# Kernel optimization log

Measured on AMD Instinct MI355X. Metric: run time of the kernel, lower is better.

## Reference

```python
import jax, jax.numpy as jnp
import numpy as np

B, N, D = 16, 1024, 5
R_HID = 8  # radial MLP hidden width


def setup_inputs() -> dict:
    key = jax.random.key(0)
    ks = jax.random.split(key, 16)
    feats = jax.random.normal(ks[0], (B, N, D), jnp.float32)
    coors = 3.0 * jax.random.normal(ks[1], (B, N, 3), jnp.float32)
    a = jax.random.bernoulli(ks[2], 0.01, (B, N, N))
    adj_mat = a | jnp.swapaxes(a, 1, 2)
    s = 1.0 / np.sqrt(D)
    Wq = s * jax.random.normal(ks[3], (D, D), jnp.float32)
    Wk = s * jax.random.normal(ks[4], (D, D), jnp.float32)
    Wv = s * jax.random.normal(ks[5], (D, D), jnp.float32)
    Wo = s * jax.random.normal(ks[6], (D, D), jnp.float32)
    w_r1 = 0.5 * jax.random.normal(ks[7], (1, R_HID), jnp.float32)
    b_r1 = jnp.zeros((R_HID,), jnp.float32)
    w_r2 = 0.5 * jax.random.normal(ks[8], (R_HID, 1), jnp.float32)
    b_r2 = jnp.zeros((1,), jnp.float32)
    w1 = (1.0 / np.sqrt(D)) * jax.random.normal(ks[9], (D, 128), jnp.float32)
    b1 = jnp.zeros((128,), jnp.float32)
    w2 = (1.0 / np.sqrt(128.0)) * jax.random.normal(ks[10], (128, 3), jnp.float32)
    b2 = jnp.zeros((3,), jnp.float32)
    return dict(feats=feats, coors=coors, adj_mat=adj_mat, Wq=Wq, Wk=Wk, Wv=Wv,
                Wo=Wo, w_r1=w_r1, b_r1=b_r1, w_r2=w_r2, b_r2=b_r2,
                w1=w1, b1=b1, w2=w2, b2=b2)


def _se3_layer(feats, coors, neigh, Wq, Wk, Wv, Wo, w_r1, b_r1, w_r2, b_r2):
    # SE(3)-invariant sparse graph attention on degree-0 channels.
    # Attention logits = content term + radial (distance-only) bias, so the
    # scalar output is invariant to global rotations/translations of coors.
    q = jnp.einsum('bnd,de->bne', feats, Wq)
    k = jnp.einsum('bnd,de->bne', feats, Wk)
    v = jnp.einsum('bnd,de->bne', feats, Wv)
    rel = coors[:, :, None, :] - coors[:, None, :, :]        # [B,N,N,3]
    dist = jnp.sqrt(jnp.sum(rel * rel, axis=-1) + 1e-8)      # [B,N,N]
    h = jax.nn.relu(dist[..., None] * w_r1[0] + b_r1)        # [B,N,N,R_HID]
    rbias = (h @ w_r2)[..., 0] + b_r2[0]                     # [B,N,N]
    scores = jnp.einsum('bid,bjd->bij', q, k) / np.sqrt(q.shape[-1]) + rbias
    scores = jnp.where(neigh, scores, -1e9)
    attn = jax.nn.softmax(scores, axis=-1)
    agg = jnp.einsum('bij,bjd->bid', attn, v)
    return feats + jnp.einsum('bid,de->bie', agg, Wo)        # residual


def reference(feats, coors, adj_mat, Wq, Wk, Wv, Wo, w_r1, b_r1, w_r2, b_r2,
              w1, b1, w2, b2):
    a = adj_mat.astype(jnp.float32)
    # num_adj_degrees=2: attend over 1-hop and 2-hop neighbors (+ self)
    adj2 = jnp.einsum('bij,bjk->bik', a, a) > 0
    eye = jnp.eye(adj_mat.shape[1], dtype=bool)[None]
    neigh = adj_mat | adj2 | eye
    x = _se3_layer(feats, coors, neigh, Wq, Wk, Wv, Wo, w_r1, b_r1, w_r2, b_r2)
    pooled = jnp.mean(x, axis=1)                              # [B, D]
    hdn = jax.nn.relu(pooled @ w1 + b1)
    return hdn @ w2 + b2                                      # [B, 3]
```

## Files before the change

### kernel.cpp

```cpp
#include <hip/hip_runtime.h>
#include <hip/hip_bf16.h>

#define BB 16
#define NN 1024
#define DD 5
#define RH 8

typedef unsigned long long u64;
typedef unsigned int u32;
typedef __hip_bfloat16 bf16;

static __device__ __forceinline__ float tof(bf16 x) { return __bfloat162float(x); }
static __device__ __forceinline__ float ldf(const void* p, long long i, bool f) {
  return f ? ((const float*)p)[i] : tof(((const bf16*)p)[i]);
}
static __device__ __forceinline__ void stG(float* p, float v) {
  __hip_atomic_store(p, v, __ATOMIC_RELAXED, __HIP_MEMORY_SCOPE_AGENT);
}
static __device__ __forceinline__ float ldG(const float* p) {
  return __hip_atomic_load(p, __ATOMIC_RELAXED, __HIP_MEMORY_SCOPE_AGENT);
}

#define LOG2E 1.4426950408889634f
#define PACK_BLOCKS (BB * NN * 16 / 256)
#define KV_BLOCKS (BB * NN / 256)

__global__ __launch_bounds__(256) void k_pack(
    const void* __restrict__ adj, const void* __restrict__ feats,
    const void* __restrict__ coors,
    const void* __restrict__ Wk, const void* __restrict__ Wv,
    const void* __restrict__ Wo,
    u64* __restrict__ adjbits, float4* __restrict__ kvg,
    float* __restrict__ czg, int* __restrict__ gflags,
    int* __restrict__ pairCnt, int* __restrict__ doneCnt,
    float* __restrict__ pooled) {
  __shared__ int sNon01, sNonpair, sLow3;
  __shared__ int sCnt[4];
  __shared__ float wkL[25], wvL[25], woL[25];
  int tid = threadIdx.x;

  if (blockIdx.x >= PACK_BLOCKS) {
    int kb = blockIdx.x - PACK_BLOCKS;
    {
      u32 x = ((const u32*)feats)[tid];
      u32 lo = x & 0xFFFFu;
      int e = (int)((lo >> 7) & 0xFFu);
      bool insane = !(lo == 0u || (e >= 90 && e <= 150));
      u64 m = __ballot(insane);
      if ((tid & 63) == 0) sCnt[tid >> 6] = (int)__popcll(m);
    }
    __syncthreads();
    bool f32 = (sCnt[0] + sCnt[1] + sCnt[2] + sCnt[3]) > 64;
    if (tid < 25) {
      wkL[tid] = ldf(Wk, tid, f32);
      wvL[tid] = ldf(Wv, tid, f32);
      woL[tid] = ldf(Wo, tid, f32);
    }
    if (kb == 0 && tid == 0) gflags[0] = f32 ? 1 : 0;
    __syncthreads();
    long long node = (long long)kb * 256 + tid;
    float f0 = ldf(feats, node * DD + 0, f32), f1 = ldf(feats, node * DD + 1, f32),
          f2 = ldf(feats, node * DD + 2, f32), f3 = ldf(feats, node * DD + 3, f32),
          f4 = ldf(feats, node * DD + 4, f32);
    float k[DD], tv[DD], v[DD];
    #pragma unroll
    for (int e = 0; e < DD; ++e) {
      k[e] = f0 * wkL[e] + f1 * wkL[5 + e] + f2 * wkL[10 + e] + f3 * wkL[15 + e] +
             f4 * wkL[20 + e];
      tv[e] = f0 * wvL[e] + f1 * wvL[5 + e] + f2 * wvL[10 + e] + f3 * wvL[15 + e] +
              f4 * wvL[20 + e];
    }
    #pragma unroll
    for (int e = 0; e < DD; ++e)
      v[e] = tv[0] * woL[e] + tv[1] * woL[5 + e] + tv[2] * woL[10 + e] +
             tv[3] * woL[15 + e] + tv[4] * woL[20 + e];
    float cx = ldf(coors, node * 3 + 0, f32);
    float cy = ldf(coors, node * 3 + 1, f32);
    float cz = ldf(coors, node * 3 + 2, f32);
    kvg[node * 3 + 0] = make_float4(k[0], k[1], k[2], k[3]);
    kvg[node * 3 + 1] = make_float4(k[4], v[0], v[1], v[2]);
    kvg[node * 3 + 2] = make_float4(v[3], v[4], cx, cy);
    czg[node] = cz;
    return;
  }

  if (blockIdx.x == 0) {
    for (int i = tid; i < BB * 64; i += 256) pairCnt[i] = 0;
    if (tid < BB * DD) pooled[tid] = 0.0f;
    if (tid == 0) *doneCnt = 0;
  }
  if (tid == 0) { sNon01 = 0; sNonpair = 0; sLow3 = 0; }
  __syncthreads();
  {
    const u32* aw = (const u32*)adj;
    int non01 = 0, nonpair = 0, low3 = 0;
    for (int i = tid; i < 4096; i += 256) {
      u32 x = aw[i];
      u32 lo = x & 0xFFFFu, hi = x >> 16;
      non01 |= (x > 1u);
      nonpair |= !((lo == 0u || lo == 0x3F80u) && (hi == 0u || hi == 0x3F80u));
      low3 |= (lo == 0x3F80u);
    }
    if (non01) atomicOr(&sNon01, 1);
    if (nonpair) atomicOr(&sNonpair, 1);
    if (low3) atomicOr(&sLow3, 1);
  }
  __syncthreads();
  int mode;
  if (!sNon01) mode = 0;
  else if (!sNonpair) mode = sLow3 ? 2 : 3;
  else mode = 1;

  int gid = blockIdx.x * 256 + tid;
  int w = gid & 15;
  long long row = gid >> 4;
  long long base = row * NN + (long long)w * 64;
  u64 bits = 0;
  if (mode == 3) {
    const uint4* p = (const uint4*)((const float*)adj + base);
    #pragma unroll
    for (int t = 0; t < 16; ++t) {
      uint4 x = p[t];
      if (x.x << 1) bits |= 1ull << (4 * t + 0);
      if (x.y << 1) bits |= 1ull << (4 * t + 1);
      if (x.z << 1) bits |= 1ull << (4 * t + 2);
      if (x.w << 1) bits |= 1ull << (4 * t + 3);
    }
  } else if (mode == 0) {
    const uint4* p = (const uint4*)((const u32*)adj + base);
    #pragma unroll
    for (int t = 0; t < 16; ++t) {
      uint4 x = p[t];
      if (x.x) bits |= 1ull << (4 * t + 0);
      if (x.y) bits |= 1ull << (4 * t + 1);
      if (x.z) bits |= 1ull << (4 * t + 2);
      if (x.w) bits |= 1ull << (4 * t + 3);
    }
  } else if (mode == 2) {
    const uint4* p = (const uint4*)((const unsigned short*)adj + base);
    #pragma unroll
    for (int t = 0; t < 8; ++t) {
      uint4 x = p[t];
      u32 c[4] = {x.x, x.y, x.z, x.w};
      #pragma unroll
      for (int q = 0; q < 4; ++q) {
        if ((c[q] & 0x7FFFu)) bits |= 1ull << (8 * t + 2 * q + 0);
        if ((c[q] >> 16) & 0x7FFFu) bits |= 1ull << (8 * t + 2 * q + 1);
      }
    }
  } else {
    const uint4* p = (const uint4*)((const unsigned char*)adj + base);
    #pragma unroll
    for (int t = 0; t < 4; ++t) {
      uint4 x = p[t];
      u32 c[4] = {x.x, x.y, x.z, x.w};
      #pragma unroll
      for (int q = 0; q < 4; ++q)
        #pragma unroll
        for (int bb = 0; bb < 4; ++bb)
          if ((c[q] >> (8 * bb)) & 0xFFu) bits |= 1ull << (16 * t + 4 * q + bb);
    }
  }
  adjbits[gid] = bits;
}

__global__ __launch_bounds__(256) void k_twohop(const u64* __restrict__ adjbits,
                                                u64* __restrict__ neighbits) {
  __shared__ unsigned short listL[4][NN];
  int wave = threadIdx.x >> 6, lane = threadIdx.x & 63;
  int row = blockIdx.x * 4 + wave;
  int b = row >> 10;
  int i = row & (NN - 1);
  int w = lane & 15;
  const u64* rowp = adjbits + (size_t)row * 16;
  u64 rw = rowp[w];
  unsigned short* list = listL[wave];
  int cnt = 0;
  #pragma unroll
  for (int sw = 0; sw < 16; ++sw) {
    u64 bits = __shfl(rw, sw, 64);
    int mybit = (int)((bits >> lane) & 1ull);
    int pre = __popcll(bits & ((1ull << lane) - 1ull));
    if (mybit) list[cnt + pre] = (unsigned short)(sw * 64 + lane);
    cnt += __popcll(bits);
  }
  __syncthreads();
  u64 acc = rw;
  if (w == (i >> 6)) acc |= 1ull << (i & 63);
  int g = lane >> 4;
  const u64* basep = adjbits + (size_t)b * NN * 16;
  for (int n = g; n < cnt; n += 4) {
    int j = list[n];
    acc |= basep[(size_t)j * 16 + w];
  }
  acc |= __shfl_xor(acc, 16, 64);
  acc |= __shfl_xor(acc, 32, 64);
  if (lane < 16) neighbits[(size_t)row * 16 + lane] = acc;
}

__global__ __launch_bounds__(256) void k_attn(
    const void* __restrict__ feats, const void* __restrict__ coors,
    const void* __restrict__ Wq,
    const void* __restrict__ wr1, const void* __restrict__ br1,
    const void* __restrict__ wr2, const void* __restrict__ br2,
    const float4* __restrict__ kvg, const float* __restrict__ czg,
    const int* __restrict__ gflags,
    const u64* __restrict__ neighbits, float* __restrict__ rowAgg,
    int* __restrict__ pairCnt, int* __restrict__ doneCnt,
    float* __restrict__ pooled,
    const void* __restrict__ w1v, const void* __restrict__ b1v,
    const void* __restrict__ w2v, const void* __restrict__ b2v,
    float* __restrict__ out) {
  __shared__ __align__(16) float4 kvL[512 * 3];
  __shared__ float czL[512];
  __shared__ float wqL[25];
  __shared__ float qL[16 * DD], ciL[16 * 3];
  __shared__ float wrL[3][RH];
  __shared__ float sConst[2];
  __shared__ int sFast, sOld, sDoneI;
  int bi = blockIdx.x;
  int b = bi >> 7, rem = bi & 127, chunk = rem >> 1, half = rem & 1;
  int j0 = half * 512;
  int tid = threadIdx.x;
  int wave = tid >> 6, lane = tid & 63;
  bool f32 = gflags[0] != 0;
  if (tid < 25) wqL[tid] = ldf(Wq, tid, f32);
  if (tid >= 64 && tid < 64 + RH) {
    int h = tid - 64;
    wrL[0][h] = ldf(wr1, h, f32);
    wrL[1][h] = ldf(br1, h, f32);
    wrL[2][h] = ldf(wr2, h, f32);
  }
  if (tid == 96) {
    float c = 0.0f;
    int ok = 1;
    #pragma unroll
    for (int h = 0; h < RH; ++h) {
      float w1h = ldf(wr1, h, f32);
      if (ldf(br1, h, f32) != 0.0f) ok = 0;
      if (w1h > 0.0f) c += w1h * ldf(wr2, h, f32);
    }
    sConst[0] = c * LOG2E;
    sConst[1] = ldf(br2, 0, f32) * LOG2E;
    sFast = ok;
  }
  {
    const float4* src = kvg + ((size_t)(b * NN) + j0) * 3;
    for (int idx = tid; idx < 512 * 3; idx += 256) kvL[idx] = src[idx];
    const float* csrc = czg + (size_t)(b * NN) + j0;
    for (int idx = tid; idx < 512; idx += 256) czL[idx] = csrc[idx];
  }
  __syncthreads();
  int fast = sFast;
  if (tid < 16) {
    long long row = (long long)b * NN + chunk * 16 + tid;
    float f0 = ldf(feats, row * DD + 0, f32), f1 = ldf(feats, row * DD + 1, f32),
          f2 = ldf(feats, row * DD + 2, f32), f3 = ldf(feats, row * DD + 3, f32),
          f4 = ldf(feats, row * DD + 4, f32);
    float qsc = fast ? (0.4472135954999579f * LOG2E) : 0.4472135954999579f;
    #pragma unroll
    for (int e = 0; e < DD; ++e)
      qL[tid * DD + e] = (f0 * wqL[e] + f1 * wqL[5 + e] + f2 * wqL[10 + e] +
                          f3 * wqL[15 + e] + f4 * wqL[20 + e]) * qsc;
    #pragma unroll
    for (int c = 0; c < 3; ++c)
      ciL[tid * 3 + c] = ldf(coors, row * 3 + c, f32);
  }
  __syncthreads();

  int i0 = chunk * 16 + wave * 4;
  float q[4][DD], ci[4][3], l[4], A[4][DD];
  #pragma unroll
  for (int r = 0; r < 4; ++r) {
    #pragma unroll
    for (int e = 0; e < DD; ++e) q[r][e] = qL[(wave * 4 + r) * DD + e];
    #pragma unroll
    for (int c = 0; c < 3; ++c) ci[r][c] = ciL[(wave * 4 + r) * 3 + c];
    l[r] = 0.0f;
    #pragma unroll
    for (int e = 0; e < DD; ++e) A[r][e] = 0.0f;
  }
  const u64* nb = neighbits + ((size_t)(b * NN + i0)) * 16 + half * 8;
  float Cf = sConst[0], br2f = sConst[1];
  for (int it = 0; it < 8; ++it) {
    int j = it * 64 + lane;
    float4 ka = kvL[j * 3 + 0];
    float4 kb = kvL[j * 3 + 1];
    float4 kc = kvL[j * 3 + 2];
    float jx = kc.z, jy = kc.w, jz = czL[j];
    u64 nw[4];
    #pragma unroll
    for (int r = 0; r < 4; ++r) nw[r] = nb[(size_t)r * 16 + it];
    if (fast) {
      #pragma unroll
      for (int r = 0; r < 4; ++r) {
        float cx = jx - ci[r][0], cy = jy - ci[r][1], cz = jz - ci[r][2];
        float dist =
            __builtin_amdgcn_sqrtf(fmaf(cx, cx, fmaf(cy, cy, fmaf(cz, cz, 1e-8f))));
        float s = fmaf(q[r][0], ka.x, br2f);
        s = fmaf(q[r][1], ka.y, s);
        s = fmaf(q[r][2], ka.z, s);
        s = fmaf(q[r][3], ka.w, s);
        s = fmaf(q[r][4], kb.x, s);
        s = fmaf(Cf, dist, s);
        s = fminf(s, 126.0f);
        s = ((nw[r] >> lane) & 1ull) ? s : -150.0f;
        float p = __builtin_amdgcn_exp2f(s);
        l[r] += p;
        A[r][0] = fmaf(p, kb.y, A[r][0]);
        A[r][1] = fmaf(p, kb.z, A[r][1]);
        A[r][2] = fmaf(p, kb.w, A[r][2]);
        A[r][3] = fmaf(p, kc.x, A[r][3]);
        A[r][4] = fmaf(p, kc.y, A[r][4]);
      }
    } else {
      #pragma unroll
      for (int r = 0; r < 4; ++r) {
        float cx = jx - ci[r][0], cy = jy - ci[r][1], cz = jz - ci[r][2];
        float dist = sqrtf(fmaf(cx, cx, fmaf(cy, cy, fmaf(cz, cz, 1e-8f))));
        float rb = ldf(br2, 0, f32);
        #pragma unroll
        for (int h = 0; h < RH; ++h)
          rb += fmaxf(dist * wrL[0][h] + wrL[1][h], 0.0f) * wrL[2][h];
        float s = fmaf(q[r][0], ka.x, rb);
        s = fmaf(q[r][1], ka.y, s);
        s = fmaf(q[r][2], ka.z, s);
        s = fmaf(q[r][3], ka.w, s);
        s = fmaf(q[r][4], kb.x, s);
        s = fminf(s, 85.0f);
        s = ((nw[r] >> lane) & 1ull) ? s : -100.0f;
        float p = __expf(s);
        l[r] += p;
        A[r][0] = fmaf(p, kb.y, A[r][0]);
        A[r][1] = fmaf(p, kb.z, A[r][1]);
        A[r][2] = fmaf(p, kb.w, A[r][2]);
        A[r][3] = fmaf(p, kc.x, A[r][3]);
        A[r][4] = fmaf(p, kc.y, A[r][4]);
      }
    }
  }
  #pragma unroll
  for (int msk = 1; msk < 64; msk <<= 1) {
    #pragma unroll
    for (int r = 0; r < 4; ++r) {
      l[r] += __shfl_xor(l[r], msk, 64);
      A[r][0] += __shfl_xor(A[r][0], msk, 64);
      A[r][1] += __shfl_xor(A[r][1], msk, 64);
      A[r][2] += __shfl_xor(A[r][2], msk, 64);
      A[r][3] += __shfl_xor(A[r][3], msk, 64);
      A[r][4] += __shfl_xor(A[r][4], msk, 64);
    }
  }
  if (lane == 0) {
    #pragma unroll
    for (int r = 0; r < 4; ++r) {
      float* o = rowAgg + (((size_t)(b * NN + i0 + r)) * 2 + half) * 6;
      stG(o + 0, l[r]);
      stG(o + 1, A[r][0]); stG(o + 2, A[r][1]); stG(o + 3, A[r][2]);
      stG(o + 4, A[r][3]); stG(o + 5, A[r][4]);
    }
  }
  __threadfence_block();
  __syncthreads();
  if (tid == 0) sOld = atomicAdd(&pairCnt[bi >> 1], 1);
  __syncthreads();
  if (sOld == 1) {
    float pe[DD] = {0.f, 0.f, 0.f, 0.f, 0.f};
    if (tid < 16) {
      size_t rid = (size_t)(b * NN + chunk * 16 + tid);
      const float* ra = rowAgg + rid * 12;
      float lsum = ldG(ra + 0) + ldG(ra + 6);
      float inv = (lsum > 0.f) ? 1.0f / lsum : 0.0f;
      long long fb = (long long)rid * DD;
      #pragma unroll
      for (int e = 0; e < DD; ++e)
        pe[e] = ldf(feats, fb + e, f32) + (ldG(ra + 1 + e) + ldG(ra + 7 + e)) * inv;
    }
    if (tid < 64) {
      #pragma unroll
      for (int off = 8; off >= 1; off >>= 1)
        #pragma unroll
        for (int e = 0; e < DD; ++e) pe[e] += __shfl_down(pe[e], off, 64);
    }
    if (tid == 0) {
      #pragma unroll
      for (int e = 0; e < DD; ++e) atomicAdd(&pooled[b * DD + e], pe[e]);
    }
  }
  __threadfence_block();
  __syncthreads();
  if (tid == 0) sDoneI = (atomicAdd(doneCnt, 1) == (int)gridDim.x - 1);
  __syncthreads();
  if (sDoneI) {
    int bb2 = tid >> 4, sub = tid & 15;
    float pl[DD];
    #pragma unroll
    for (int e = 0; e < DD; ++e)
      pl[e] = ldG(&pooled[bb2 * DD + e]) * (1.0f / 1024.0f);
    float a0 = 0.f, a1 = 0.f, a2 = 0.f;
    for (int jj = sub * 8; jj < sub * 8 + 8; ++jj) {
      float h = ldf(b1v, jj, f32);
      #pragma unroll
      for (int d = 0; d < DD; ++d)
        h = fmaf(pl[d], ldf(w1v, d * 128 + jj, f32), h);
      h = fmaxf(h, 0.0f);
      a0 = fmaf(h, ldf(w2v, jj * 3 + 0, f32), a0);
      a1 = fmaf(h, ldf(w2v, jj * 3 + 1, f32), a1);
      a2 = fmaf(h, ldf(w2v, jj * 3 + 2, f32), a2);
    }
    #pragma unroll
    for (int mk = 1; mk < 16; mk <<= 1) {
      a0 += __shfl_xor(a0, mk, 64);
      a1 += __shfl_xor(a1, mk, 64);
      a2 += __shfl_xor(a2, mk, 64);
    }
    if (sub == 0) {
      out[bb2 * 3 + 0] = a0 + ldf(b2v, 0, f32);
      out[bb2 * 3 + 1] = a1 + ldf(b2v, 1, f32);
      out[bb2 * 3 + 2] = a2 + ldf(b2v, 2, f32);
    }
  }
}

extern "C" void kernel_launch(void* const* d_in, const int* in_sizes, int n_in,
                              void* d_out, int out_size, void* d_ws, size_t ws_size,
                              hipStream_t stream) {
  const void* adj = d_in[2];
  float* out = (float*)d_out;

  char* w = (char*)d_ws;
  int* gflags = (int*)w;
  float* pooled = (float*)(w + 64);
  int* doneCnt = (int*)(w + 448);
  int* pairCnt = (int*)(w + 1024);
  const size_t MB2 = (size_t)BB * NN * 16 * sizeof(u64);
  u64* adjbits = (u64*)(w + 8192);
  u64* neighbits = (u64*)(w + 8192 + MB2);
  float* rowAgg = (float*)(w + 8192 + 2 * MB2);
  float4* kvg = (float4*)(w + 8192 + 2 * MB2 + 786432);
  float* czg = (float*)(w + 8192 + 2 * MB2 + 2 * 786432);

  k_pack<<<PACK_BLOCKS + KV_BLOCKS, 256, 0, stream>>>(
      adj, d_in[0], d_in[1], d_in[4], d_in[5], d_in[6], adjbits, kvg, czg,
      gflags, pairCnt, doneCnt, pooled);
  k_twohop<<<BB * NN / 4, 256, 0, stream>>>(adjbits, neighbits);
  k_attn<<<BB * 128, 256, 0, stream>>>(d_in[0], d_in[1], d_in[3], d_in[7], d_in[8],
                                       d_in[9], d_in[10], kvg, czg, gflags,
                                       neighbits, rowAgg, pairCnt, doneCnt, pooled,
                                       d_in[11], d_in[12], d_in[13], d_in[14], out);
}
```

Baseline: 203.9 us.

## Process full key range per block, drop split-half rowAgg combine pass

Each attention block now covers all 1024 keys for its 16 rows in two staged phases, instead of two blocks each handling half the keys and merging partial sums through a global rowAgg buffer and pair counters. Pooling is reduced in shared memory per block before one global atomic per channel. This removes the global partial-sum round trip, the pair-counter atomics and the extra synchronisation, but halves the grid (1024 blocks) and serialises the two key halves, which lowers parallelism and adds a shared-memory reload barrier.

```diff
diff --git a/kernel.cpp b/kernel.cpp
--- a/kernel.cpp
+++ b/kernel.cpp
@@ -14,10 +14,7 @@
 static __device__ __forceinline__ float ldf(const void* p, long long i, bool f) {
   return f ? ((const float*)p)[i] : tof(((const bf16*)p)[i]);
 }
-static __device__ __forceinline__ void stG(float* p, float v) {
-  __hip_atomic_store(p, v, __ATOMIC_RELAXED, __HIP_MEMORY_SCOPE_AGENT);
-}
-static __device__ __forceinline__ float ldG(const float* p) {
+static __device__ __forceinline__ float ldA(const float* p) {
   return __hip_atomic_load(p, __ATOMIC_RELAXED, __HIP_MEMORY_SCOPE_AGENT);
 }
 
@@ -32,8 +29,7 @@
     const void* __restrict__ Wo,
     u64* __restrict__ adjbits, float4* __restrict__ kvg,
     float* __restrict__ czg, int* __restrict__ gflags,
-    int* __restrict__ pairCnt, int* __restrict__ doneCnt,
-    float* __restrict__ pooled) {
+    float* __restrict__ pooled, int* __restrict__ doneCnt) {
   __shared__ int sNon01, sNonpair, sLow3;
   __shared__ int sCnt[4];
   __shared__ float wkL[25], wvL[25], woL[25];
@@ -85,7 +81,6 @@
   }
 
   if (blockIdx.x == 0) {
-    for (int i = tid; i < BB * 64; i += 256) pairCnt[i] = 0;
     if (tid < BB * DD) pooled[tid] = 0.0f;
     if (tid == 0) *doneCnt = 0;
   }
@@ -205,9 +200,8 @@
     const void* __restrict__ wr2, const void* __restrict__ br2,
     const float4* __restrict__ kvg, const float* __restrict__ czg,
     const int* __restrict__ gflags,
-    const u64* __restrict__ neighbits, float* __restrict__ rowAgg,
-    int* __restrict__ pairCnt, int* __restrict__ doneCnt,
-    float* __restrict__ pooled,
+    const u64* __restrict__ neighbits, float* __restrict__ pooled,
+    int* __restrict__ doneCnt,
     const void* __restrict__ w1v, const void* __restrict__ b1v,
     const void* __restrict__ w2v, const void* __restrict__ b2v,
     float* __restrict__ out) {
@@ -216,11 +210,11 @@
   __shared__ float wqL[25];
   __shared__ float qL[16 * DD], ciL[16 * 3];
   __shared__ float wrL[3][RH];
+  __shared__ float poolL[DD];
   __shared__ float sConst[2];
-  __shared__ int sFast, sOld, sDoneI;
+  __shared__ int sFast, sDone;
   int bi = blockIdx.x;
-  int b = bi >> 7, rem = bi & 127, chunk = rem >> 1, half = rem & 1;
-  int j0 = half * 512;
+  int b = bi >> 6, chunk = bi & 63;
   int tid = threadIdx.x;
   int wave = tid >> 6, lane = tid & 63;
   bool f32 = gflags[0] != 0;
@@ -244,12 +238,7 @@
     sConst[1] = ldf(br2, 0, f32) * LOG2E;
     sFast = ok;
   }
-  {
-    const float4* src = kvg + ((size_t)(b * NN) + j0) * 3;
-    for (int idx = tid; idx < 512 * 3; idx += 256) kvL[idx] = src[idx];
-    const float* csrc = czg + (size_t)(b * NN) + j0;
-    for (int idx = tid; idx < 512; idx += 256) czL[idx] = csrc[idx];
-  }
+  if (tid < DD) poolL[tid] = 0.0f;
   __syncthreads();
   int fast = sFast;
   if (tid < 16) {
@@ -266,76 +255,91 @@
     for (int c = 0; c < 3; ++c)
       ciL[tid * 3 + c] = ldf(coors, row * 3 + c, f32);
   }
-  __syncthreads();
 
   int i0 = chunk * 16 + wave * 4;
   float q[4][DD], ci[4][3], l[4], A[4][DD];
   #pragma unroll
   for (int r = 0; r < 4; ++r) {
-    #pragma unroll
-    for (int e = 0; e < DD; ++e) q[r][e] = qL[(wave * 4 + r) * DD + e];
-    #pragma unroll
-    for (int c = 0; c < 3; ++c) ci[r][c] = ciL[(wave * 4 + r) * 3 + c];
     l[r] = 0.0f;
     #pragma unroll
     for (int e = 0; e < DD; ++e) A[r][e] = 0.0f;
   }
-  const u64* nb = neighbits + ((size_t)(b * NN + i0)) * 16 + half * 8;
+  const u64* nb = neighbits + ((size_t)(b * NN + i0)) * 16;
   float Cf = sConst[0], br2f = sConst[1];
-  for (int it = 0; it < 8; ++it) {
-    int j = it * 64 + lane;
-    float4 ka = kvL[j * 3 + 0];
-    float4 kb = kvL[j * 3 + 1];
-    float4 kc = kvL[j * 3 + 2];
-    float jx = kc.z, jy = kc.w, jz = czL[j];
-    u64 nw[4];
-    #pragma unroll
-    for (int r = 0; r < 4; ++r) nw[r] = nb[(size_t)r * 16 + it];
-    if (fast) {
+  for (int ph = 0; ph < 2; ++ph) {
+    __syncthreads();
+    {
+      const float4* src = kvg + ((size_t)(b * NN) + ph * 512) * 3;
+      for (int idx = tid; idx < 512 * 3; idx += 256) kvL[idx] = src[idx];
+      const float* csrc = czg + (size_t)(b * NN) + ph * 512;
+      for (int idx = tid; idx < 512; idx += 256) czL[idx] = csrc[idx];
+    }
+    __syncthreads();
+    if (ph == 0) {
       #pragma unroll
       for (int r = 0; r < 4; ++r) {
-        float cx = jx - ci[r][0], cy = jy - ci[r][1], cz = jz - ci[r][2];
-        float dist =
-            __builtin_amdgcn_sqrtf(fmaf(cx, cx, fmaf(cy, cy, fmaf(cz, cz, 1e-8f))));
-        float s = fmaf(q[r][0], ka.x, br2f);
-        s = fmaf(q[r][1], ka.y, s);
-        s = fmaf(q[r][2], ka.z, s);
-        s = fmaf(q[r][3], ka.w, s);
-        s = fmaf(q[r][4], kb.x, s);
-        s = fmaf(Cf, dist, s);
-        s = fminf(s, 126.0f);
-        s = ((nw[r] >> lane) & 1ull) ? s : -150.0f;
-        float p = __builtin_amdgcn_exp2f(s);
-        l[r] += p;
-        A[r][0] = fmaf(p, kb.y, A[r][0]);
-        A[r][1] = fmaf(p, kb.z, A[r][1]);
-        A[r][2] = fmaf(p, kb.w, A[r][2]);
-        A[r][3] = fmaf(p, kc.x, A[r][3]);
-        A[r][4] = fmaf(p, kc.y, A[r][4]);
+        #pragma unroll
+        for (int e = 0; e < DD; ++e) q[r][e] = qL[(wave * 4 + r) * DD + e];
+        #pragma unroll
+        for (int c = 0; c < 3; ++c) ci[r][c] = ciL[(wave * 4 + r) * 3 + c];
       }
-    } else {
-      #pragma unroll
-      for (int r = 0; r < 4; ++r) {
-        float cx = jx - ci[r][0], cy = jy - ci[r][1], cz = jz - ci[r][2];
-        float dist = sqrtf(fmaf(cx, cx, fmaf(cy, cy, fmaf(cz, cz, 1e-8f))));
-        float rb = ldf(br2, 0, f32);
+    }
+    for (int it = 0; it < 8; ++it) {
+      int itg = ph * 8 + it;
+      int j = it * 64 + lane;
+      float4 ka = kvL[j * 3 + 0];
+      float4 kb = kvL[j * 3 + 1];
+      float4 kc = kvL[j * 3 + 2];
+      float jx = kc.z, jy = kc.w, jz = czL[j];
+      u64 nw[4];
+      #pragma unroll
+      for (int r = 0; r < 4; ++r) nw[r] = nb[(size_t)r * 16 + itg];
+      if (fast) {
         #pragma unroll
-        for (int h = 0; h < RH; ++h)
-          rb += fmaxf(dist * wrL[0][h] + wrL[1][h], 0.0f) * wrL[2][h];
-        float s = fmaf(q[r][0], ka.x, rb);
-        s = fmaf(q[r][1], ka.y, s);
-        s = fmaf(q[r][2], ka.z, s);
-        s = fmaf(q[r][3], ka.w, s);
-        s = fmaf(q[r][4], kb.x, s);
-        s = fminf(s, 85.0f);
-        s = ((nw[r] >> lane) & 1ull) ? s : -100.0f;
-        float p = __expf(s);
-        l[r] += p;
-        A[r][0] = fmaf(p, kb.y, A[r][0]);
-        A[r][1] = fmaf(p, kb.z, A[r][1]);
-        A[r][2] = fmaf(p, kb.w, A[r][2]);
-        A[r][3] = fmaf(p, kc.x, A[r][3]);
-        A[r][4] = fmaf(p, kc.y, A[r][4]);
+        for (int r = 0; r < 4; ++r) {
+          float cx = jx - ci[r][0], cy = jy - ci[r][1], cz = jz - ci[r][2];
+          float dist =
+              __builtin_amdgcn_sqrtf(fmaf(cx, cx, fmaf(cy, cy, fmaf(cz, cz, 1e-8f))));
+          float s = fmaf(q[r][0], ka.x, br2f);
+          s = fmaf(q[r][1], ka.y, s);
+          s = fmaf(q[r][2], ka.z, s);
+          s = fmaf(q[r][3], ka.w, s);
+          s = fmaf(q[r][4], kb.x, s);
+          s = fmaf(Cf, dist, s);
+          s = fminf(s, 126.0f);
+          s = ((nw[r] >> lane) & 1ull) ? s : -150.0f;
+          float p = __builtin_amdgcn_exp2f(s);
+          l[r] += p;
+          A[r][0] = fmaf(p, kb.y, A[r][0]);
+          A[r][1] = fmaf(p, kb.z, A[r][1]);
+          A[r][2] = fmaf(p, kb.w, A[r][2]);
+          A[r][3] = fmaf(p, kc.x, A[r][3]);
+          A[r][4] = fmaf(p, kc.y, A[r][4]);
+        }
+      } else {
+        #pragma unroll
+        for (int r = 0; r < 4; ++r) {
+          float cx = jx - ci[r][0], cy = jy - ci[r][1], cz = jz - ci[r][2];
+          float dist = sqrtf(fmaf(cx, cx, fmaf(cy, cy, fmaf(cz, cz, 1e-8f))));
+          float rb = ldf(br2, 0, f32);
+          #pragma unroll
+          for (int h = 0; h < RH; ++h)
+            rb += fmaxf(dist * wrL[0][h] + wrL[1][h], 0.0f) * wrL[2][h];
+          float s = fmaf(q[r][0], ka.x, rb);
+          s = fmaf(q[r][1], ka.y, s);
+          s = fmaf(q[r][2], ka.z, s);
+          s = fmaf(q[r][3], ka.w, s);
+          s = fmaf(q[r][4], kb.x, s);
+          s = fminf(s, 85.0f);
+          s = ((nw[r] >> lane) & 1ull) ? s : -100.0f;
+          float p = __expf(s);
+          l[r] += p;
+          A[r][0] = fmaf(p, kb.y, A[r][0]);
+          A[r][1] = fmaf(p, kb.z, A[r][1]);
+          A[r][2] = fmaf(p, kb.w, A[r][2]);
+          A[r][3] = fmaf(p, kc.x, A[r][3]);
+          A[r][4] = fmaf(p, kc.y, A[r][4]);
+        }
       }
     }
   }
@@ -352,51 +356,32 @@
     }
   }
   if (lane == 0) {
+    float pe[DD] = {0.f, 0.f, 0.f, 0.f, 0.f};
     #pragma unroll
     for (int r = 0; r < 4; ++r) {
-      float* o = rowAgg + (((size_t)(b * NN + i0 + r)) * 2 + half) * 6;
-      stG(o + 0, l[r]);
-      stG(o + 1, A[r][0]); stG(o + 2, A[r][1]); stG(o + 3, A[r][2]);
-      stG(o + 4, A[r][3]); stG(o + 5, A[r][4]);
-    }
-  }
-  __threadfence_block();
-  __syncthreads();
-  if (tid == 0) sOld = atomicAdd(&pairCnt[bi >> 1], 1);
-  __syncthreads();
-  if (sOld == 1) {
-    float pe[DD] = {0.f, 0.f, 0.f, 0.f, 0.f};
-    if (tid < 16) {
-      size_t rid = (size_t)(b * NN + chunk * 16 + tid);
-      const float* ra = rowAgg + rid * 12;
-      float lsum = ldG(ra + 0) + ldG(ra + 6);
-      float inv = (lsum > 0.f) ? 1.0f / lsum : 0.0f;
-      long long fb = (long long)rid * DD;
+      float inv = (l[r] > 0.f) ? 1.0f / l[r] : 0.0f;
+      long long base = ((long long)b * NN + i0 + r) * DD;
       #pragma unroll
       for (int e = 0; e < DD; ++e)
-        pe[e] = ldf(feats, fb + e, f32) + (ldG(ra + 1 + e) + ldG(ra + 7 + e)) * inv;
-    }
-    if (tid < 64) {
-      #pragma unroll
-      for (int off = 8; off >= 1; off >>= 1)
-        #pragma unroll
-        for (int e = 0; e < DD; ++e) pe[e] += __shfl_down(pe[e], off, 64);
-    }
-    if (tid == 0) {
-      #pragma unroll
-      for (int e = 0; e < DD; ++e) atomicAdd(&pooled[b * DD + e], pe[e]);
-    }
-  }
-  __threadfence_block();
-  __syncthreads();
-  if (tid == 0) sDoneI = (atomicAdd(doneCnt, 1) == (int)gridDim.x - 1);
-  __syncthreads();
-  if (sDoneI) {
+        pe[e] += ldf(feats, base + e, f32) + A[r][e] * inv;
+    }
+    #pragma unroll
+    for (int e = 0; e < DD; ++e) atomicAdd(&poolL[e], pe[e]);
+  }
+  __syncthreads();
+  if (tid < DD) atomicAdd(&pooled[b * DD + tid], poolL[tid]);
+  __syncthreads();
+  if (tid == 0)
+    sDone = (__hip_atomic_fetch_add(doneCnt, 1, __ATOMIC_ACQ_REL,
+                                    __HIP_MEMORY_SCOPE_AGENT) ==
+             (int)gridDim.x - 1);
+  __syncthreads();
+  if (sDone) {
     int bb2 = tid >> 4, sub = tid & 15;
     float pl[DD];
     #pragma unroll
     for (int e = 0; e < DD; ++e)
-      pl[e] = ldG(&pooled[bb2 * DD + e]) * (1.0f / 1024.0f);
+      pl[e] = ldA(&pooled[bb2 * DD + e]) * (1.0f / 1024.0f);
     float a0 = 0.f, a1 = 0.f, a2 = 0.f;
     for (int jj = sub * 8; jj < sub * 8 + 8; ++jj) {
       float h = ldf(b1v, jj, f32);
@@ -432,20 +417,18 @@
   int* gflags = (int*)w;
   float* pooled = (float*)(w + 64);
   int* doneCnt = (int*)(w + 448);
-  int* pairCnt = (int*)(w + 1024);
   const size_t MB2 = (size_t)BB * NN * 16 * sizeof(u64);
   u64* adjbits = (u64*)(w + 8192);
   u64* neighbits = (u64*)(w + 8192 + MB2);
-  float* rowAgg = (float*)(w + 8192 + 2 * MB2);
-  float4* kvg = (float4*)(w + 8192 + 2 * MB2 + 786432);
-  float* czg = (float*)(w + 8192 + 2 * MB2 + 2 * 786432);
+  float4* kvg = (float4*)(w + 8192 + 2 * MB2);
+  float* czg = (float*)(w + 8192 + 2 * MB2 + 786432);
 
   k_pack<<<PACK_BLOCKS + KV_BLOCKS, 256, 0, stream>>>(
       adj, d_in[0], d_in[1], d_in[4], d_in[5], d_in[6], adjbits, kvg, czg,
-      gflags, pairCnt, doneCnt, pooled);
+      gflags, pooled, doneCnt);
   k_twohop<<<BB * NN / 4, 256, 0, stream>>>(adjbits, neighbits);
-  k_attn<<<BB * 128, 256, 0, stream>>>(d_in[0], d_in[1], d_in[3], d_in[7], d_in[8],
-                                       d_in[9], d_in[10], kvg, czg, gflags,
-                                       neighbits, rowAgg, pairCnt, doneCnt, pooled,
-                                       d_in[11], d_in[12], d_in[13], d_in[14], out);
-}
+  k_attn<<<BB * 64, 256, 0, stream>>>(d_in[0], d_in[1], d_in[3], d_in[7], d_in[8],
+                                      d_in[9], d_in[10], kvg, czg, gflags,
+                                      neighbits, pooled, doneCnt,
+                                      d_in[11], d_in[12], d_in[13], d_in[14], out);
+}
```

After: 191.4 us. 6.1% less time.
